# Kernel optimization log

Hardware: AMD Instinct MI355X
Metric: run time of the kernel (lower is better)

The kernel has to match this reference:

```python
import jax, jax.numpy as jnp
import numpy as np

N = 10000      # num nodes
D = 128        # in_channels == out_channels (x is fed back each step)
E1 = 320000    # edges for TAGConv
E2 = 320000    # edges for Transformer_Block
STEPS = 5      # gd_steps


def setup_inputs() -> dict:
    key = jax.random.key(0)
    ks = jax.random.split(key, 8)
    x = jax.random.normal(ks[0], (N, D), dtype=jnp.float32)
    edge_index = jax.random.randint(ks[1], (2, E1), 0, N)
    edge_index_2 = jax.random.randint(ks[2], (2, E2), 0, N)
    s = 0.02  # small init keeps the un-normalized attention unroll numerically sane
    W0 = jax.random.normal(ks[3], (D, D), dtype=jnp.float32) * s  # TAGConv lin for hop-0
    W1 = jax.random.normal(ks[4], (D, D), dtype=jnp.float32) * s  # TAGConv lin for hop-1 (A x)
    Wq = jax.random.normal(ks[5], (D, D), dtype=jnp.float32) * s
    Wk = jax.random.normal(ks[6], (D, D), dtype=jnp.float32) * s
    Wv = jax.random.normal(ks[7], (D, D), dtype=jnp.float32) * s
    return {"x": x, "edge_index": edge_index, "edge_index_2": edge_index_2,
            "W0": W0, "W1": W1, "Wq": Wq, "Wk": Wk, "Wv": Wv}


def reference(x, edge_index, edge_index_2, W0, W1, Wq, Wk, Wv):
    src, dst = edge_index[0], edge_index[1]        # message flows src -> dst
    src2, dst2 = edge_index_2[0], edge_index_2[1]

    def gd_step(h, _):
        # TAGConv(K=1, normalize=False, bias=False): W0 h + W1 (A h)
        agg = jax.ops.segment_sum(h[src], dst, num_segments=N)   # [N, D] sum over in-neighbors
        x1 = h @ W0 + agg @ W1
        # Transformer_Block (graph attention over edge_index_2, use_softmax=False):
        # alpha_ij = <q_i, k_j> on edges, out_i = sum_j alpha_ij * v_j
        Q, K, V = h @ Wq, h @ Wk, h @ Wv
        alpha = jnp.sum(Q[dst2] * K[src2], axis=-1)              # [E2] raw scores, no softmax
        x2 = jax.ops.segment_sum(alpha[:, None] * V[src2], dst2, num_segments=N)
        return x1 - x2, None

    out, _ = jax.lax.scan(gd_step, x, None, length=STEPS)
    return out
```

## Files before the change

### kernel.cpp

```cpp
#include <hip/hip_runtime.h>

#define D 128

typedef __attribute__((ext_vector_type(8))) short bf16x8;
typedef __attribute__((ext_vector_type(4))) float f32x4;

__device__ __forceinline__ unsigned short f2bf(float f) {
  union { float f; unsigned int u; } c; c.f = f;
  unsigned int u = c.u;
  unsigned int r = (u + 0x7fffu + ((u >> 16) & 1u)) >> 16;
  return (unsigned short)r;
}
__device__ __forceinline__ float bf2f(unsigned short h) {
  return __uint_as_float(((unsigned int)h) << 16);
}
__device__ __forceinline__ float bf_lo(unsigned int w) {
  return __uint_as_float(w << 16);
}
__device__ __forceinline__ float bf_hi(unsigned int w) {
  return __uint_as_float(w & 0xffff0000u);
}
__device__ __forceinline__ void split2(float a, float b, unsigned int& hi, unsigned int& lo) {
  unsigned short ha = f2bf(a), hb = f2bf(b);
  unsigned short la = f2bf(a - bf2f(ha)), lb = f2bf(b - bf2f(hb));
  hi = (unsigned int)ha | ((unsigned int)hb << 16);
  lo = (unsigned int)la | ((unsigned int)lb << 16);
}

__device__ __forceinline__ void frag_write(unsigned short* __restrict__ Afh,
                                           unsigned short* __restrict__ Afl,
                                           int t, int r, int k, float a, float b) {
  unsigned int hh, hl;
  split2(a, b, hh, hl);
  int s = k >> 5, ksub = (k & 31) >> 3, e = k & 7;
  size_t addr = ((size_t)(t * 12 + s) * 64 + r + 16 * ksub) * 8 + e;
  *(unsigned int*)&Afh[addr] = hh;
  *(unsigned int*)&Afl[addr] = hl;
}


__global__ void hist2_k(const int* __restrict__ dst1, int* __restrict__ c1, int E1,
                        const int* __restrict__ dst2, int* __restrict__ c2, int E2) {
  int e = blockIdx.x * blockDim.x + threadIdx.x;
  if (e < E1) atomicAdd(&c1[dst1[e]], 1);
  int e2 = e - E1;
  if (e2 >= 0 && e2 < E2) atomicAdd(&c2[dst2[e2]], 1);
}

__device__ void exscan_dev(int* cnt_cursor, int* rp, int n) {
  __shared__ int wsum[16];
  __shared__ int carry_s;
  const int tid = threadIdx.x;
  const int lane = tid & 63, wid = tid >> 6;
  if (tid == 0) carry_s = 0;
  __syncthreads();
  for (int base = 0; base < n; base += 1024) {
    int idx = base + tid;
    int v = (idx < n) ? cnt_cursor[idx] : 0;
    int s = v;
#pragma unroll
    for (int ofs = 1; ofs < 64; ofs <<= 1) {
      int t = __shfl_up(s, ofs);
      if (lane >= ofs) s += t;
    }
    if (lane == 63) wsum[wid] = s;
    __syncthreads();
    if (wid == 0) {
      int ws = (lane < 16) ? wsum[lane] : 0;
#pragma unroll
      for (int ofs = 1; ofs < 16; ofs <<= 1) {
        int t = __shfl_up(ws, ofs);
        if (lane >= ofs) ws += t;
      }
      if (lane < 16) wsum[lane] = ws;
    }
    __syncthreads();
    int pre = (wid > 0) ? wsum[wid - 1] : 0;
    int carry = carry_s;
    int ex = carry + pre + s - v;
    if (idx < n) { rp[idx] = ex; cnt_cursor[idx] = ex; }
    __syncthreads();
    if (tid == 1023) carry_s = carry + wsum[15];
    __syncthreads();
  }
  if (tid == 0) rp[n] = carry_s;
}

__global__ void exscan2_k(int* c1, int* r1, int* c2, int* r2, int n) {
  if (blockIdx.x == 0) exscan_dev(c1, r1, n);
  else exscan_dev(c2, r2, n);
}

__global__ void fill2_k(const int* __restrict__ src1, const int* __restrict__ dst1,
                        int* __restrict__ cur1, int* __restrict__ out1, int E1,
                        const int* __restrict__ src2, const int* __restrict__ dst2,
                        int* __restrict__ cur2, int* __restrict__ out2, int E2) {
  int e = blockIdx.x * blockDim.x + threadIdx.x;
  if (e < E1) {
    int pos = atomicAdd(&cur1[dst1[e]], 1);
    out1[pos] = src1[e];
  }
  int e2 = e - E1;
  if (e2 >= 0 && e2 < E2) {
    int pos = atomicAdd(&cur2[dst2[e2]], 1);
    out2[pos] = src2[e2];
  }
}

__global__ __launch_bounds__(256) void pre1_k(
    const float* __restrict__ Wq, const float* __restrict__ Wk,
    const float* __restrict__ W0, const float* __restrict__ W1,
    const float* __restrict__ Wv,
    float* __restrict__ M, float* __restrict__ Wc,
    int* __restrict__ cur, int twoN) {
  int gid = blockIdx.x * 256 + threadIdx.x;
  if (gid < twoN) cur[gid] = 0;
  int bx = blockIdx.x;
  if (bx < 64) {
    int r = bx * 2 + (threadIdx.x >> 7);
    int c = threadIdx.x & 127;
    float acc = 0.f;
    for (int d = 0; d < D; ++d) acc += Wq[r * D + d] * Wk[c * D + d];
    M[r * D + c] = acc;
  } else {
    int idx = (bx - 64) * 256 + threadIdx.x;
    int r = idx >> 7, c = idx & 127;
    float v;
    if (r < 128) v = W0[r * D + c];
    else if (r < 256) v = W1[(r - 128) * D + c];
    else v = -Wv[(r - 256) * D + c];
    Wc[idx] = v;
  }
}

__global__ __launch_bounds__(256) void pre2_k(const float* __restrict__ Wc,
                                              const float* __restrict__ M,
                                              float* __restrict__ WM) {
  int idx = blockIdx.x * blockDim.x + threadIdx.x;
  if (idx >= 384 * D) return;
  int r = idx >> 7, c = idx & 127;
  float acc = 0.f;
  for (int k = 0; k < D; ++k) acc += Wc[r * D + k] * M[k * D + c];
  WM[idx] = acc;
}

__global__ __launch_bounds__(256) void pre3cvt_k(
    const float* __restrict__ x,
    unsigned short* __restrict__ Afh, unsigned short* __restrict__ Afl,
    unsigned short* __restrict__ Hb, int ncvt,
    const float* __restrict__ Wc, const float* __restrict__ WM,
    const float* __restrict__ M,
    unsigned short* __restrict__ Bfh, unsigned short* __restrict__ Bfl,
    unsigned short* __restrict__ Mfh, unsigned short* __restrict__ Mfl) {
  int gid = blockIdx.x * blockDim.x + threadIdx.x;
  if (gid < ncvt) {
    int row = gid >> 6, f = (gid & 63) * 2;
    float2 v = *(const float2*)&x[row * D + f];
    frag_write(Afh, Afl, row >> 4, row & 15, f, v.x, v.y);
    unsigned int p = (unsigned int)f2bf(v.x) | ((unsigned int)f2bf(v.y) << 16);
    *(unsigned int*)&Hb[(size_t)row * D + f] = p;
    return;
  }
  int idx = gid - ncvt;
  if (idx < 16 * 12 * 512) {
    int e = idx & 7, l = (idx >> 3) & 63;
    int s = (idx >> 9) % 12, ntg = idx / (12 * 512);
    int n = ntg * 16 + (l & 15);
    int k = s * 32 + (l >> 4) * 8 + e;
    float v = (n < 128) ? Wc[k * D + n] : WM[k * D + (n - 128)];
    unsigned short h = f2bf(v);
    Bfh[idx] = h;
    Bfl[idx] = f2bf(v - bf2f(h));
  } else {
    int i2 = idx - 16 * 12 * 512;
    if (i2 >= 8 * 4 * 512) return;
    int e = i2 & 7, l = (i2 >> 3) & 63;
    int s = (i2 >> 9) & 3, ntg = i2 / (4 * 512);
    int n = ntg * 16 + (l & 15);
    int k = s * 32 + (l >> 4) * 8 + e;
    float v = M[k * D + n];
    unsigned short h = f2bf(v);
    Mfh[i2] = h;
    Mfl[i2] = f2bf(v - bf2f(h));
  }
}

__global__ __launch_bounds__(256) void agg_k(
    const float* __restrict__ h, int ldh,
    const float* __restrict__ qt,
    const unsigned short* __restrict__ Hb,
    const int* __restrict__ rp1, const int* __restrict__ s1,
    const int* __restrict__ rp2, const int* __restrict__ s2,
    unsigned short* __restrict__ Afh, unsigned short* __restrict__ Afl, int N) {
  int gw = (int)((blockIdx.x * blockDim.x + threadIdx.x) >> 6);
  if (gw >= N) return;
  const int i = __builtin_amdgcn_readfirstlane(gw);
  const int l = threadIdx.x & 63;
  const int m = l & 15, g = l >> 4;
  const int c0 = m * 8;

  float q[8];
  *(float4*)&q[0] = *(const float4*)&qt[(size_t)i * 256 + c0];
  *(float4*)&q[4] = *(const float4*)&qt[(size_t)i * 256 + c0 + 4];

  float a1[8] = {0.f, 0.f, 0.f, 0.f, 0.f, 0.f, 0.f, 0.f};
  float a2[8] = {0.f, 0.f, 0.f, 0.f, 0.f, 0.f, 0.f, 0.f};

  {
    const int lo = rp1[i], end = rp1[i + 1];
    bool nv0 = false, nv1 = false;
    int nj0 = 0, nj1 = 0;
    if (lo < end) {
      nv0 = lo + g < end;      nj0 = nv0 ? s1[lo + g] : 0;
      nv1 = lo + 4 + g < end;  nj1 = nv1 ? s1[lo + 4 + g] : 0;
    }
    for (int e = lo; e < end; e += 8) {
      int j0 = nj0, j1 = nj1;
      bool v0 = nv0, v1 = nv1;
      int en = e + 8;
      if (en < end) {
        nv0 = en + g < end;      nj0 = nv0 ? s1[en + g] : 0;
        nv1 = en + 4 + g < end;  nj1 = nv1 ? s1[en + 4 + g] : 0;
      }
      uint4 w0 = *(const uint4*)&Hb[(size_t)j0 * D + c0];
      uint4 w1 = *(const uint4*)&Hb[(size_t)j1 * D + c0];
      if (!v0) w0 = make_uint4(0u, 0u, 0u, 0u);
      if (!v1) w1 = make_uint4(0u, 0u, 0u, 0u);
      a1[0] += bf_lo(w0.x) + bf_lo(w1.x); a1[1] += bf_hi(w0.x) + bf_hi(w1.x);
      a1[2] += bf_lo(w0.y) + bf_lo(w1.y); a1[3] += bf_hi(w0.y) + bf_hi(w1.y);
      a1[4] += bf_lo(w0.z) + bf_lo(w1.z); a1[5] += bf_hi(w0.z) + bf_hi(w1.z);
      a1[6] += bf_lo(w0.w) + bf_lo(w1.w); a1[7] += bf_hi(w0.w) + bf_hi(w1.w);
    }
  }

  {
    const int lo = rp2[i], end = rp2[i + 1];
    bool nv0 = false, nv1 = false;
    int nj0 = 0, nj1 = 0;
    if (lo < end) {
      nv0 = lo + g < end;      nj0 = nv0 ? s2[lo + g] : 0;
      nv1 = lo + 4 + g < end;  nj1 = nv1 ? s2[lo + 4 + g] : 0;
    }
    for (int e = lo; e < end; e += 8) {
      int j0 = nj0, j1 = nj1;
      bool v0 = nv0, v1 = nv1;
      int en = e + 8;
      if (en < end) {
        nv0 = en + g < end;      nj0 = nv0 ? s2[en + g] : 0;
        nv1 = en + 4 + g < end;  nj1 = nv1 ? s2[en + 4 + g] : 0;
      }
      uint4 w0 = *(const uint4*)&Hb[(size_t)j0 * D + c0];
      uint4 w1 = *(const uint4*)&Hb[(size_t)j1 * D + c0];
      if (!v0) w0 = make_uint4(0u, 0u, 0u, 0u);
      if (!v1) w1 = make_uint4(0u, 0u, 0u, 0u);
      float f0[8], f1[8];
      f0[0] = bf_lo(w0.x); f0[1] = bf_hi(w0.x); f0[2] = bf_lo(w0.y); f0[3] = bf_hi(w0.y);
      f0[4] = bf_lo(w0.z); f0[5] = bf_hi(w0.z); f0[6] = bf_lo(w0.w); f0[7] = bf_hi(w0.w);
      f1[0] = bf_lo(w1.x); f1[1] = bf_hi(w1.x); f1[2] = bf_lo(w1.y); f1[3] = bf_hi(w1.y);
      f1[4] = bf_lo(w1.z); f1[5] = bf_hi(w1.z); f1[6] = bf_lo(w1.w); f1[7] = bf_hi(w1.w);
      float p0 = q[0] * f0[0] + q[1] * f0[1] + q[2] * f0[2] + q[3] * f0[3] +
                 q[4] * f0[4] + q[5] * f0[5] + q[6] * f0[6] + q[7] * f0[7];
      float p1 = q[0] * f1[0] + q[1] * f1[1] + q[2] * f1[2] + q[3] * f1[3] +
                 q[4] * f1[4] + q[5] * f1[5] + q[6] * f1[6] + q[7] * f1[7];
#pragma unroll
      for (int ofs = 1; ofs < 16; ofs <<= 1) {
        p0 += __shfl_xor(p0, ofs);
        p1 += __shfl_xor(p1, ofs);
      }
#pragma unroll
      for (int t = 0; t < 8; ++t) a2[t] += p0 * f0[t] + p1 * f1[t];
    }
  }

#pragma unroll
  for (int t = 0; t < 8; ++t) {
    a1[t] += __shfl_xor(a1[t], 16); a1[t] += __shfl_xor(a1[t], 32);
    a2[t] += __shfl_xor(a2[t], 16); a2[t] += __shfl_xor(a2[t], 32);
  }

  if (g < 3) {
    float vals[8];
    if (g == 0) {
      *(float4*)&vals[0] = *(const float4*)&h[(size_t)i * ldh + c0];
      *(float4*)&vals[4] = *(const float4*)&h[(size_t)i * ldh + c0 + 4];
    } else if (g == 1) {
#pragma unroll
      for (int t = 0; t < 8; ++t) vals[t] = a1[t];
    } else {
#pragma unroll
      for (int t = 0; t < 8; ++t) vals[t] = a2[t];
    }
    uint4 hiw, low;
    split2(vals[0], vals[1], hiw.x, low.x);
    split2(vals[2], vals[3], hiw.y, low.y);
    split2(vals[4], vals[5], hiw.z, low.z);
    split2(vals[6], vals[7], hiw.w, low.w);
    size_t base = (((size_t)(i >> 4) * 12 + g * 4 + (m >> 2)) * 64 +
                   (i & 15) + 16 * (m & 3)) * 8;
    *(uint4*)&Afh[base] = hiw;
    *(uint4*)&Afl[base] = low;
  }
}

__global__ __launch_bounds__(256) void gemm_mfma(
    const unsigned short* __restrict__ Afh, const unsigned short* __restrict__ Afl,
    int ksteps,
    const unsigned short* __restrict__ Bfh, const unsigned short* __restrict__ Bfl,
    int outcol0, float* __restrict__ C, int ldc,
    unsigned short* __restrict__ Hb,
    int N, int ntiles, int log2ny) {
  const int w = threadIdx.x >> 6, l = threadIdx.x & 63;
  const int wr = w & 1, wc = w >> 1;

  const int nwg = gridDim.x;
  const int flat = blockIdx.x;
  const int xcd = flat & 7;
  const int qq = nwg >> 3, rr8 = nwg & 7;
  const int wgid = (xcd < rr8 ? xcd * (qq + 1) : rr8 * (qq + 1) + (xcd - rr8) * qq) + (flat >> 3);
  const int rowblk = wgid >> log2ny;
  const int panel = wgid - (rowblk << log2ny);

  const int rowbase = rowblk * 64 + wr * 32;
  const int ntg0 = panel * 4 + wc * 2;

  int t_[2];
#pragma unroll
  for (int tr = 0; tr < 2; ++tr) {
    int t = (rowbase >> 4) + tr;
    t_[tr] = (t < ntiles) ? t : (ntiles - 1);
  }

  const size_t loff = (size_t)l * 8;
  const unsigned short* ah[2];
  const unsigned short* al[2];
#pragma unroll
  for (int tr = 0; tr < 2; ++tr) {
    ah[tr] = Afh + (size_t)t_[tr] * 12 * 512 + loff;
    al[tr] = Afl + (size_t)t_[tr] * 12 * 512 + loff;
  }
  const unsigned short* bh[2];
  const unsigned short* bl[2];
#pragma unroll
  for (int nt = 0; nt < 2; ++nt) {
    bh[nt] = Bfh + (size_t)(ntg0 + nt) * ksteps * 512 + loff;
    bl[nt] = Bfl + (size_t)(ntg0 + nt) * ksteps * 512 + loff;
  }

  f32x4 acc[2][2] = {};
  for (int s = 0; s < ksteps; ++s) {
    bf16x8 Ah[2], Al[2], Bh[2], Bl[2];
#pragma unroll
    for (int tr = 0; tr < 2; ++tr) {
      Ah[tr] = *(const bf16x8*)(ah[tr] + (size_t)s * 512);
      Al[tr] = *(const bf16x8*)(al[tr] + (size_t)s * 512);
    }
#pragma unroll
    for (int nt = 0; nt < 2; ++nt) {
      Bh[nt] = *(const bf16x8*)(bh[nt] + (size_t)s * 512);
      Bl[nt] = *(const bf16x8*)(bl[nt] + (size_t)s * 512);
    }
#pragma unroll
    for (int nt = 0; nt < 2; ++nt) {
#pragma unroll
      for (int tr = 0; tr < 2; ++tr) {
        acc[tr][nt] = __builtin_amdgcn_mfma_f32_16x16x32_bf16(Ah[tr], Bh[nt], acc[tr][nt], 0, 0, 0);
        acc[tr][nt] = __builtin_amdgcn_mfma_f32_16x16x32_bf16(Ah[tr], Bl[nt], acc[tr][nt], 0, 0, 0);
        acc[tr][nt] = __builtin_amdgcn_mfma_f32_16x16x32_bf16(Al[tr], Bh[nt], acc[tr][nt], 0, 0, 0);
      }
    }
  }

  const int r4 = 4 * (l >> 4), cc = (l & 15);
#pragma unroll
  for (int tr = 0; tr < 2; ++tr) {
#pragma unroll
    for (int nt = 0; nt < 2; ++nt) {
      int col = outcol0 + (ntg0 + nt) * 16 + cc;
#pragma unroll
      for (int rr = 0; rr < 4; ++rr) {
        int row = rowbase + tr * 16 + r4 + rr;
        if (row < N) {
          float v = acc[tr][nt][rr];
          C[(size_t)row * ldc + col] = v;
          if (Hb && col < 128) Hb[(size_t)row * D + col] = f2bf(v);
        }
      }
    }
  }
}


extern "C" void kernel_launch(void* const* d_in, const int* in_sizes, int n_in,
                              void* d_out, int out_size, void* d_ws, size_t ws_size,
                              hipStream_t stream) {
  const float* x  = (const float*)d_in[0];
  const int* ei1  = (const int*)d_in[1];
  const int* ei2  = (const int*)d_in[2];
  const float* W0 = (const float*)d_in[3];
  const float* W1 = (const float*)d_in[4];
  const float* Wq = (const float*)d_in[5];
  const float* Wk = (const float*)d_in[6];
  const float* Wv = (const float*)d_in[7];

  const int N  = in_sizes[0] / D;
  const int E1 = in_sizes[1] / 2;
  const int E2 = in_sizes[2] / 2;
  const int* src1 = ei1;
  const int* dst1 = ei1 + E1;
  const int* src2 = ei2;
  const int* dst2 = ei2 + E2;
  const int TILES = (N + 15) / 16;

  float* Cbuf = (float*)d_ws;
  float* M    = Cbuf + (size_t)N * 256;
  float* Wc   = M + 16384;
  float* WM   = Wc + 49152;
  unsigned short* Afh = (unsigned short*)(WM + 49152);
  unsigned short* Afl = Afh + (size_t)TILES * 6144;
  unsigned short* Bfh = Afl + (size_t)TILES * 6144;
  unsigned short* Bfl = Bfh + 98304;
  unsigned short* Mfh = Bfl + 98304;
  unsigned short* Mfl = Mfh + 16384;
  unsigned short* Hb  = Mfl + 16384;
  int* rp1   = (int*)(Hb + (size_t)N * D);
  int* rp2   = rp1 + (N + 1);
  int* cur1  = rp2 + (N + 1);
  int* cur2  = cur1 + N;
  int* srcs1 = cur2 + N;
  int* srcs2 = srcs1 + E1;

  size_t needed = ((size_t)N * 256 + 16384 + 2 * 49152) * 4ull +
                  ((size_t)2 * TILES * 6144 + 2 * 98304 + 2 * 16384 + (size_t)N * D) * 2ull +
                  ((size_t)2 * (N + 1) + 2ull * N + E1 + E2) * 4ull;
  if (ws_size < needed) return;

  float* out = (float*)d_out;

  pre1_k<<<256, 256, 0, stream>>>(Wq, Wk, W0, W1, Wv, M, Wc, cur1, 2 * N);
  pre2_k<<<(384 * D + 255) / 256, 256, 0, stream>>>(Wc, M, WM);
  {
    int ncvt = N * 64;
    int tot = ncvt + 16 * 12 * 512 + 8 * 4 * 512;
    pre3cvt_k<<<(tot + 255) / 256, 256, 0, stream>>>(x, Afh, Afl, Hb, ncvt,
                                                     Wc, WM, M, Bfh, Bfl, Mfh, Mfl);
  }
  int ebt = (E1 + E2 + 255) / 256;
  hist2_k<<<ebt, 256, 0, stream>>>(dst1, cur1, E1, dst2, cur2, E2);
  exscan2_k<<<2, 1024, 0, stream>>>(cur1, rp1, cur2, rp2, N);
  fill2_k<<<ebt, 256, 0, stream>>>(src1, dst1, cur1, srcs1, E1,
                                   src2, dst2, cur2, srcs2, E2);

  const int gx = (N + 63) / 64;
  const int ablocks = (N * 64 + 255) / 256;

  gemm_mfma<<<gx * 2, 256, 0, stream>>>(Afh, Afl, 4, Mfh, Mfl,
                                        128, Cbuf, 256, nullptr, N, TILES, 1);

  for (int s = 0; s < 5; ++s) {
    const float* hsrc = (s == 0) ? x : Cbuf;
    const int ldh = (s == 0) ? D : 256;

    agg_k<<<ablocks, 256, 0, stream>>>(hsrc, ldh, Cbuf + 128, Hb,
                                       rp1, srcs1, rp2, srcs2, Afh, Afl, N);

    if (s == 4) {
      gemm_mfma<<<gx * 2, 256, 0, stream>>>(Afh, Afl, 12, Bfh, Bfl,
                                            0, out, D, nullptr, N, TILES, 1);
    } else {
      gemm_mfma<<<gx * 4, 256, 0, stream>>>(Afh, Afl, 12, Bfh, Bfl,
                                            0, Cbuf, 256, Hb, N, TILES, 2);
    }
  }
}
```

Measured before the change: 313.5 us.

## Merge setup kernels into fewer launches and unroll edge gathers by four

The preprocessing chain goes from seven launches to four. Independent work now shares a launch: histogram with the W*M product, prefix scans with the bf16 fragment conversion, and CSR fill with the initial Q-projection GEMM, which is pulled out into a shared device function. This cuts launch and serialization overhead between small dependent kernels. Separately, the aggregation kernel now gathers four neighbor rows per iteration instead of two, exposing more memory-level parallelism at some cost in register pressure.

```diff
diff --git a/kernel.cpp b/kernel.cpp
--- a/kernel.cpp
+++ b/kernel.cpp
@@ -38,14 +38,6 @@
   *(unsigned int*)&Afl[addr] = hl;
 }
 
-
-__global__ void hist2_k(const int* __restrict__ dst1, int* __restrict__ c1, int E1,
-                        const int* __restrict__ dst2, int* __restrict__ c2, int E2) {
-  int e = blockIdx.x * blockDim.x + threadIdx.x;
-  if (e < E1) atomicAdd(&c1[dst1[e]], 1);
-  int e2 = e - E1;
-  if (e2 >= 0 && e2 < E2) atomicAdd(&c2[dst2[e2]], 1);
-}
 
 __device__ void exscan_dev(int* cnt_cursor, int* rp, int n) {
   __shared__ int wsum[16];
@@ -86,28 +78,86 @@
   if (tid == 0) rp[n] = carry_s;
 }
 
-__global__ void exscan2_k(int* c1, int* r1, int* c2, int* r2, int n) {
-  if (blockIdx.x == 0) exscan_dev(c1, r1, n);
-  else exscan_dev(c2, r2, n);
-}
-
-__global__ void fill2_k(const int* __restrict__ src1, const int* __restrict__ dst1,
-                        int* __restrict__ cur1, int* __restrict__ out1, int E1,
-                        const int* __restrict__ src2, const int* __restrict__ dst2,
-                        int* __restrict__ cur2, int* __restrict__ out2, int E2) {
-  int e = blockIdx.x * blockDim.x + threadIdx.x;
-  if (e < E1) {
-    int pos = atomicAdd(&cur1[dst1[e]], 1);
-    out1[pos] = src1[e];
-  }
-  int e2 = e - E1;
-  if (e2 >= 0 && e2 < E2) {
-    int pos = atomicAdd(&cur2[dst2[e2]], 1);
-    out2[pos] = src2[e2];
-  }
-}
-
-__global__ __launch_bounds__(256) void pre1_k(
+__device__ void gemm_tile(
+    const unsigned short* __restrict__ Afh, const unsigned short* __restrict__ Afl,
+    int ksteps,
+    const unsigned short* __restrict__ Bfh, const unsigned short* __restrict__ Bfl,
+    int outcol0, float* __restrict__ C, int ldc,
+    unsigned short* __restrict__ Hb, int N, int ntiles, int log2ny, int wgid) {
+  const int w = threadIdx.x >> 6, l = threadIdx.x & 63;
+  const int wr = w & 1, wc = w >> 1;
+  const int rowblk = wgid >> log2ny;
+  const int panel = wgid - (rowblk << log2ny);
+  const int rowbase = rowblk * 64 + wr * 32;
+  const int ntg0 = panel * 4 + wc * 2;
+
+  int t_[2];
+#pragma unroll
+  for (int tr = 0; tr < 2; ++tr) {
+    int t = (rowbase >> 4) + tr;
+    t_[tr] = (t < ntiles) ? t : (ntiles - 1);
+  }
+
+  const size_t loff = (size_t)l * 8;
+  const unsigned short* ah[2];
+  const unsigned short* al[2];
+#pragma unroll
+  for (int tr = 0; tr < 2; ++tr) {
+    ah[tr] = Afh + (size_t)t_[tr] * 12 * 512 + loff;
+    al[tr] = Afl + (size_t)t_[tr] * 12 * 512 + loff;
+  }
+  const unsigned short* bh[2];
+  const unsigned short* bl[2];
+#pragma unroll
+  for (int nt = 0; nt < 2; ++nt) {
+    bh[nt] = Bfh + (size_t)(ntg0 + nt) * ksteps * 512 + loff;
+    bl[nt] = Bfl + (size_t)(ntg0 + nt) * ksteps * 512 + loff;
+  }
+
+  f32x4 acc[2][2] = {};
+  for (int s = 0; s < ksteps; ++s) {
+    bf16x8 Ah[2], Al[2], Bh[2], Bl[2];
+#pragma unroll
+    for (int tr = 0; tr < 2; ++tr) {
+      Ah[tr] = *(const bf16x8*)(ah[tr] + (size_t)s * 512);
+      Al[tr] = *(const bf16x8*)(al[tr] + (size_t)s * 512);
+    }
+#pragma unroll
+    for (int nt = 0; nt < 2; ++nt) {
+      Bh[nt] = *(const bf16x8*)(bh[nt] + (size_t)s * 512);
+      Bl[nt] = *(const bf16x8*)(bl[nt] + (size_t)s * 512);
+    }
+#pragma unroll
+    for (int nt = 0; nt < 2; ++nt) {
+#pragma unroll
+      for (int tr = 0; tr < 2; ++tr) {
+        acc[tr][nt] = __builtin_amdgcn_mfma_f32_16x16x32_bf16(Ah[tr], Bh[nt], acc[tr][nt], 0, 0, 0);
+        acc[tr][nt] = __builtin_amdgcn_mfma_f32_16x16x32_bf16(Ah[tr], Bl[nt], acc[tr][nt], 0, 0, 0);
+        acc[tr][nt] = __builtin_amdgcn_mfma_f32_16x16x32_bf16(Al[tr], Bh[nt], acc[tr][nt], 0, 0, 0);
+      }
+    }
+  }
+
+  const int r4 = 4 * (l >> 4), cc = (l & 15);
+#pragma unroll
+  for (int tr = 0; tr < 2; ++tr) {
+#pragma unroll
+    for (int nt = 0; nt < 2; ++nt) {
+      int col = outcol0 + (ntg0 + nt) * 16 + cc;
+#pragma unroll
+      for (int rr = 0; rr < 4; ++rr) {
+        int row = rowbase + tr * 16 + r4 + rr;
+        if (row < N) {
+          float v = acc[tr][nt][rr];
+          C[(size_t)row * ldc + col] = v;
+          if (Hb && col < 128) Hb[(size_t)row * D + col] = f2bf(v);
+        }
+      }
+    }
+  }
+}
+
+__global__ __launch_bounds__(256) void k1_pre1(
     const float* __restrict__ Wq, const float* __restrict__ Wk,
     const float* __restrict__ W0, const float* __restrict__ W1,
     const float* __restrict__ Wv,
@@ -133,18 +183,28 @@
   }
 }
 
-__global__ __launch_bounds__(256) void pre2_k(const float* __restrict__ Wc,
-                                              const float* __restrict__ M,
-                                              float* __restrict__ WM) {
-  int idx = blockIdx.x * blockDim.x + threadIdx.x;
-  if (idx >= 384 * D) return;
-  int r = idx >> 7, c = idx & 127;
-  float acc = 0.f;
-  for (int k = 0; k < D; ++k) acc += Wc[r * D + k] * M[k * D + c];
-  WM[idx] = acc;
-}
-
-__global__ __launch_bounds__(256) void pre3cvt_k(
+__global__ __launch_bounds__(256) void k2_hist_pre2(
+    const int* __restrict__ dst1, int* __restrict__ c1, int E1,
+    const int* __restrict__ dst2, int* __restrict__ c2, int E2, int ebt,
+    const float* __restrict__ Wc, const float* __restrict__ M,
+    float* __restrict__ WM) {
+  if (blockIdx.x < (unsigned)ebt) {
+    int e = blockIdx.x * 256 + threadIdx.x;
+    if (e < E1) atomicAdd(&c1[dst1[e]], 1);
+    int e2 = e - E1;
+    if (e2 >= 0 && e2 < E2) atomicAdd(&c2[dst2[e2]], 1);
+  } else {
+    int idx = (blockIdx.x - ebt) * 256 + threadIdx.x;
+    if (idx >= 384 * D) return;
+    int r = idx >> 7, c = idx & 127;
+    float acc = 0.f;
+    for (int k = 0; k < D; ++k) acc += Wc[r * D + k] * M[k * D + c];
+    WM[idx] = acc;
+  }
+}
+
+__global__ __launch_bounds__(1024) void k3_scan_pre3cvt(
+    int* c1, int* r1, int* c2, int* r2, int n,
     const float* __restrict__ x,
     unsigned short* __restrict__ Afh, unsigned short* __restrict__ Afl,
     unsigned short* __restrict__ Hb, int ncvt,
@@ -152,7 +212,9 @@
     const float* __restrict__ M,
     unsigned short* __restrict__ Bfh, unsigned short* __restrict__ Bfl,
     unsigned short* __restrict__ Mfh, unsigned short* __restrict__ Mfl) {
-  int gid = blockIdx.x * blockDim.x + threadIdx.x;
+  if (blockIdx.x == 0) { exscan_dev(c1, r1, n); return; }
+  if (blockIdx.x == 1) { exscan_dev(c2, r2, n); return; }
+  int gid = (blockIdx.x - 2) * 1024 + threadIdx.x;
   if (gid < ncvt) {
     int row = gid >> 6, f = (gid & 63) * 2;
     float2 v = *(const float2*)&x[row * D + f];
@@ -165,9 +227,9 @@
   if (idx < 16 * 12 * 512) {
     int e = idx & 7, l = (idx >> 3) & 63;
     int s = (idx >> 9) % 12, ntg = idx / (12 * 512);
-    int n = ntg * 16 + (l & 15);
+    int n2 = ntg * 16 + (l & 15);
     int k = s * 32 + (l >> 4) * 8 + e;
-    float v = (n < 128) ? Wc[k * D + n] : WM[k * D + (n - 128)];
+    float v = (n2 < 128) ? Wc[k * D + n2] : WM[k * D + (n2 - 128)];
     unsigned short h = f2bf(v);
     Bfh[idx] = h;
     Bfl[idx] = f2bf(v - bf2f(h));
@@ -176,12 +238,37 @@
     if (i2 >= 8 * 4 * 512) return;
     int e = i2 & 7, l = (i2 >> 3) & 63;
     int s = (i2 >> 9) & 3, ntg = i2 / (4 * 512);
-    int n = ntg * 16 + (l & 15);
+    int n2 = ntg * 16 + (l & 15);
     int k = s * 32 + (l >> 4) * 8 + e;
-    float v = M[k * D + n];
+    float v = M[k * D + n2];
     unsigned short h = f2bf(v);
     Mfh[i2] = h;
     Mfl[i2] = f2bf(v - bf2f(h));
+  }
+}
+
+__global__ __launch_bounds__(256) void k4_fill_qtgemm(
+    const int* __restrict__ src1, const int* __restrict__ dst1,
+    int* __restrict__ cur1, int* __restrict__ out1, int E1,
+    const int* __restrict__ src2, const int* __restrict__ dst2,
+    int* __restrict__ cur2, int* __restrict__ out2, int E2, int ebt,
+    const unsigned short* __restrict__ Afh, const unsigned short* __restrict__ Afl,
+    const unsigned short* __restrict__ Mfh, const unsigned short* __restrict__ Mfl,
+    float* __restrict__ Cbuf, int N, int ntiles) {
+  if (blockIdx.x < (unsigned)ebt) {
+    int e = blockIdx.x * 256 + threadIdx.x;
+    if (e < E1) {
+      int pos = atomicAdd(&cur1[dst1[e]], 1);
+      out1[pos] = src1[e];
+    }
+    int e2 = e - E1;
+    if (e2 >= 0 && e2 < E2) {
+      int pos = atomicAdd(&cur2[dst2[e2]], 1);
+      out2[pos] = src2[e2];
+    }
+  } else {
+    gemm_tile(Afh, Afl, 4, Mfh, Mfl, 128, Cbuf, 256, nullptr, N, ntiles, 1,
+              blockIdx.x - ebt);
   }
 }
 
@@ -208,67 +295,83 @@
 
   {
     const int lo = rp1[i], end = rp1[i + 1];
-    bool nv0 = false, nv1 = false;
-    int nj0 = 0, nj1 = 0;
-    if (lo < end) {
-      nv0 = lo + g < end;      nj0 = nv0 ? s1[lo + g] : 0;
-      nv1 = lo + 4 + g < end;  nj1 = nv1 ? s1[lo + 4 + g] : 0;
-    }
-    for (int e = lo; e < end; e += 8) {
-      int j0 = nj0, j1 = nj1;
-      bool v0 = nv0, v1 = nv1;
-      int en = e + 8;
+    int nj[4]; bool nv[4];
+#pragma unroll
+    for (int u = 0; u < 4; ++u) {
+      int ee = lo + 4 * u + g;
+      nv[u] = ee < end; nj[u] = nv[u] ? s1[ee] : 0;
+    }
+    for (int e = lo; e < end; e += 16) {
+      int j[4]; bool v[4];
+#pragma unroll
+      for (int u = 0; u < 4; ++u) { j[u] = nj[u]; v[u] = nv[u]; }
+      int en = e + 16;
       if (en < end) {
-        nv0 = en + g < end;      nj0 = nv0 ? s1[en + g] : 0;
-        nv1 = en + 4 + g < end;  nj1 = nv1 ? s1[en + 4 + g] : 0;
-      }
-      uint4 w0 = *(const uint4*)&Hb[(size_t)j0 * D + c0];
-      uint4 w1 = *(const uint4*)&Hb[(size_t)j1 * D + c0];
-      if (!v0) w0 = make_uint4(0u, 0u, 0u, 0u);
-      if (!v1) w1 = make_uint4(0u, 0u, 0u, 0u);
-      a1[0] += bf_lo(w0.x) + bf_lo(w1.x); a1[1] += bf_hi(w0.x) + bf_hi(w1.x);
-      a1[2] += bf_lo(w0.y) + bf_lo(w1.y); a1[3] += bf_hi(w0.y) + bf_hi(w1.y);
-      a1[4] += bf_lo(w0.z) + bf_lo(w1.z); a1[5] += bf_hi(w0.z) + bf_hi(w1.z);
-      a1[6] += bf_lo(w0.w) + bf_lo(w1.w); a1[7] += bf_hi(w0.w) + bf_hi(w1.w);
+#pragma unroll
+        for (int u = 0; u < 4; ++u) {
+          int ee = en + 4 * u + g;
+          nv[u] = ee < end; nj[u] = nv[u] ? s1[ee] : 0;
+        }
+      }
+      uint4 w[4];
+#pragma unroll
+      for (int u = 0; u < 4; ++u)
+        w[u] = *(const uint4*)&Hb[(size_t)j[u] * D + c0];
+#pragma unroll
+      for (int u = 0; u < 4; ++u) {
+        if (!v[u]) w[u] = make_uint4(0u, 0u, 0u, 0u);
+        a1[0] += bf_lo(w[u].x); a1[1] += bf_hi(w[u].x);
+        a1[2] += bf_lo(w[u].y); a1[3] += bf_hi(w[u].y);
+        a1[4] += bf_lo(w[u].z); a1[5] += bf_hi(w[u].z);
+        a1[6] += bf_lo(w[u].w); a1[7] += bf_hi(w[u].w);
+      }
     }
   }
 
   {
     const int lo = rp2[i], end = rp2[i + 1];
-    bool nv0 = false, nv1 = false;
-    int nj0 = 0, nj1 = 0;
-    if (lo < end) {
-      nv0 = lo + g < end;      nj0 = nv0 ? s2[lo + g] : 0;
-      nv1 = lo + 4 + g < end;  nj1 = nv1 ? s2[lo + 4 + g] : 0;
-    }
-    for (int e = lo; e < end; e += 8) {
-      int j0 = nj0, j1 = nj1;
-      bool v0 = nv0, v1 = nv1;
-      int en = e + 8;
+    int nj[4]; bool nv[4];
+#pragma unroll
+    for (int u = 0; u < 4; ++u) {
+      int ee = lo + 4 * u + g;
+      nv[u] = ee < end; nj[u] = nv[u] ? s2[ee] : 0;
+    }
+    for (int e = lo; e < end; e += 16) {
+      int j[4]; bool v[4];
+#pragma unroll
+      for (int u = 0; u < 4; ++u) { j[u] = nj[u]; v[u] = nv[u]; }
+      int en = e + 16;
       if (en < end) {
-        nv0 = en + g < end;      nj0 = nv0 ? s2[en + g] : 0;
-        nv1 = en + 4 + g < end;  nj1 = nv1 ? s2[en + 4 + g] : 0;
-      }
-      uint4 w0 = *(const uint4*)&Hb[(size_t)j0 * D + c0];
-      uint4 w1 = *(const uint4*)&Hb[(size_t)j1 * D + c0];
-      if (!v0) w0 = make_uint4(0u, 0u, 0u, 0u);
-      if (!v1) w1 = make_uint4(0u, 0u, 0u, 0u);
-      float f0[8], f1[8];
-      f0[0] = bf_lo(w0.x); f0[1] = bf_hi(w0.x); f0[2] = bf_lo(w0.y); f0[3] = bf_hi(w0.y);
-      f0[4] = bf_lo(w0.z); f0[5] = bf_hi(w0.z); f0[6] = bf_lo(w0.w); f0[7] = bf_hi(w0.w);
-      f1[0] = bf_lo(w1.x); f1[1] = bf_hi(w1.x); f1[2] = bf_lo(w1.y); f1[3] = bf_hi(w1.y);
-      f1[4] = bf_lo(w1.z); f1[5] = bf_hi(w1.z); f1[6] = bf_lo(w1.w); f1[7] = bf_hi(w1.w);
-      float p0 = q[0] * f0[0] + q[1] * f0[1] + q[2] * f0[2] + q[3] * f0[3] +
-                 q[4] * f0[4] + q[5] * f0[5] + q[6] * f0[6] + q[7] * f0[7];
-      float p1 = q[0] * f1[0] + q[1] * f1[1] + q[2] * f1[2] + q[3] * f1[3] +
-                 q[4] * f1[4] + q[5] * f1[5] + q[6] * f1[6] + q[7] * f1[7];
+#pragma unroll
+        for (int u = 0; u < 4; ++u) {
+          int ee = en + 4 * u + g;
+          nv[u] = ee < end; nj[u] = nv[u] ? s2[ee] : 0;
+        }
+      }
+      uint4 w[4];
+#pragma unroll
+      for (int u = 0; u < 4; ++u)
+        w[u] = *(const uint4*)&Hb[(size_t)j[u] * D + c0];
+      float fv[4][8]; float p[4];
+#pragma unroll
+      for (int u = 0; u < 4; ++u) {
+        if (!v[u]) w[u] = make_uint4(0u, 0u, 0u, 0u);
+        fv[u][0] = bf_lo(w[u].x); fv[u][1] = bf_hi(w[u].x);
+        fv[u][2] = bf_lo(w[u].y); fv[u][3] = bf_hi(w[u].y);
+        fv[u][4] = bf_lo(w[u].z); fv[u][5] = bf_hi(w[u].z);
+        fv[u][6] = bf_lo(w[u].w); fv[u][7] = bf_hi(w[u].w);
+        p[u] = q[0] * fv[u][0] + q[1] * fv[u][1] + q[2] * fv[u][2] + q[3] * fv[u][3] +
+               q[4] * fv[u][4] + q[5] * fv[u][5] + q[6] * fv[u][6] + q[7] * fv[u][7];
+      }
 #pragma unroll
       for (int ofs = 1; ofs < 16; ofs <<= 1) {
-        p0 += __shfl_xor(p0, ofs);
-        p1 += __shfl_xor(p1, ofs);
-      }
-#pragma unroll
-      for (int t = 0; t < 8; ++t) a2[t] += p0 * f0[t] + p1 * f1[t];
+#pragma unroll
+        for (int u = 0; u < 4; ++u) p[u] += __shfl_xor(p[u], ofs);
+      }
+#pragma unroll
+      for (int u = 0; u < 4; ++u)
+#pragma unroll
+        for (int t = 0; t < 8; ++t) a2[t] += p[u] * fv[u][t];
     }
   }
 
@@ -307,86 +410,13 @@
     int ksteps,
     const unsigned short* __restrict__ Bfh, const unsigned short* __restrict__ Bfl,
     int outcol0, float* __restrict__ C, int ldc,
-    unsigned short* __restrict__ Hb,
-    int N, int ntiles, int log2ny) {
-  const int w = threadIdx.x >> 6, l = threadIdx.x & 63;
-  const int wr = w & 1, wc = w >> 1;
-
+    unsigned short* __restrict__ Hb, int N, int ntiles, int log2ny) {
   const int nwg = gridDim.x;
   const int flat = blockIdx.x;
   const int xcd = flat & 7;
   const int qq = nwg >> 3, rr8 = nwg & 7;
   const int wgid = (xcd < rr8 ? xcd * (qq + 1) : rr8 * (qq + 1) + (xcd - rr8) * qq) + (flat >> 3);
-  const int rowblk = wgid >> log2ny;
-  const int panel = wgid - (rowblk << log2ny);
-
-  const int rowbase = rowblk * 64 + wr * 32;
-  const int ntg0 = panel * 4 + wc * 2;
-
-  int t_[2];
-#pragma unroll
-  for (int tr = 0; tr < 2; ++tr) {
-    int t = (rowbase >> 4) + tr;
-    t_[tr] = (t < ntiles) ? t : (ntiles - 1);
-  }
-
-  const size_t loff = (size_t)l * 8;
-  const unsigned short* ah[2];
-  const unsigned short* al[2];
-#pragma unroll
-  for (int tr = 0; tr < 2; ++tr) {
-    ah[tr] = Afh + (size_t)t_[tr] * 12 * 512 + loff;
-    al[tr] = Afl + (size_t)t_[tr] * 12 * 512 + loff;
-  }
-  const unsigned short* bh[2];
-  const unsigned short* bl[2];
-#pragma unroll
-  for (int nt = 0; nt < 2; ++nt) {
-    bh[nt] = Bfh + (size_t)(ntg0 + nt) * ksteps * 512 + loff;
-    bl[nt] = Bfl + (size_t)(ntg0 + nt) * ksteps * 512 + loff;
-  }
-
-  f32x4 acc[2][2] = {};
-  for (int s = 0; s < ksteps; ++s) {
-    bf16x8 Ah[2], Al[2], Bh[2], Bl[2];
-#pragma unroll
-    for (int tr = 0; tr < 2; ++tr) {
-      Ah[tr] = *(const bf16x8*)(ah[tr] + (size_t)s * 512);
-      Al[tr] = *(const bf16x8*)(al[tr] + (size_t)s * 512);
-    }
-#pragma unroll
-    for (int nt = 0; nt < 2; ++nt) {
-      Bh[nt] = *(const bf16x8*)(bh[nt] + (size_t)s * 512);
-      Bl[nt] = *(const bf16x8*)(bl[nt] + (size_t)s * 512);
-    }
-#pragma unroll
-    for (int nt = 0; nt < 2; ++nt) {
-#pragma unroll
-      for (int tr = 0; tr < 2; ++tr) {
-        acc[tr][nt] = __builtin_amdgcn_mfma_f32_16x16x32_bf16(Ah[tr], Bh[nt], acc[tr][nt], 0, 0, 0);
-        acc[tr][nt] = __builtin_amdgcn_mfma_f32_16x16x32_bf16(Ah[tr], Bl[nt], acc[tr][nt], 0, 0, 0);
-        acc[tr][nt] = __builtin_amdgcn_mfma_f32_16x16x32_bf16(Al[tr], Bh[nt], acc[tr][nt], 0, 0, 0);
-      }
-    }
-  }
-
-  const int r4 = 4 * (l >> 4), cc = (l & 15);
-#pragma unroll
-  for (int tr = 0; tr < 2; ++tr) {
-#pragma unroll
-    for (int nt = 0; nt < 2; ++nt) {
-      int col = outcol0 + (ntg0 + nt) * 16 + cc;
-#pragma unroll
-      for (int rr = 0; rr < 4; ++rr) {
-        int row = rowbase + tr * 16 + r4 + rr;
-        if (row < N) {
-          float v = acc[tr][nt][rr];
-          C[(size_t)row * ldc + col] = v;
-          if (Hb && col < 128) Hb[(size_t)row * D + col] = f2bf(v);
-        }
-      }
-    }
-  }
+  gemm_tile(Afh, Afl, ksteps, Bfh, Bfl, outcol0, C, ldc, Hb, N, ntiles, log2ny, wgid);
 }
 
 
@@ -436,25 +466,21 @@
 
   float* out = (float*)d_out;
 
-  pre1_k<<<256, 256, 0, stream>>>(Wq, Wk, W0, W1, Wv, M, Wc, cur1, 2 * N);
-  pre2_k<<<(384 * D + 255) / 256, 256, 0, stream>>>(Wc, M, WM);
-  {
-    int ncvt = N * 64;
-    int tot = ncvt + 16 * 12 * 512 + 8 * 4 * 512;
-    pre3cvt_k<<<(tot + 255) / 256, 256, 0, stream>>>(x, Afh, Afl, Hb, ncvt,
-                                                     Wc, WM, M, Bfh, Bfl, Mfh, Mfl);
-  }
-  int ebt = (E1 + E2 + 255) / 256;
-  hist2_k<<<ebt, 256, 0, stream>>>(dst1, cur1, E1, dst2, cur2, E2);
-  exscan2_k<<<2, 1024, 0, stream>>>(cur1, rp1, cur2, rp2, N);
-  fill2_k<<<ebt, 256, 0, stream>>>(src1, dst1, cur1, srcs1, E1,
-                                   src2, dst2, cur2, srcs2, E2);
-
+  const int ebt = (E1 + E2 + 255) / 256;
   const int gx = (N + 63) / 64;
   const int ablocks = (N * 64 + 255) / 256;
-
-  gemm_mfma<<<gx * 2, 256, 0, stream>>>(Afh, Afl, 4, Mfh, Mfl,
-                                        128, Cbuf, 256, nullptr, N, TILES, 1);
+  const int ncvt = N * 64;
+  const int tot3 = ncvt + 16 * 12 * 512 + 8 * 4 * 512;
+
+  k1_pre1<<<256, 256, 0, stream>>>(Wq, Wk, W0, W1, Wv, M, Wc, cur1, 2 * N);
+  k2_hist_pre2<<<ebt + 192, 256, 0, stream>>>(dst1, cur1, E1, dst2, cur2, E2, ebt,
+                                              Wc, M, WM);
+  k3_scan_pre3cvt<<<2 + (tot3 + 1023) / 1024, 1024, 0, stream>>>(
+      cur1, rp1, cur2, rp2, N, x, Afh, Afl, Hb, ncvt,
+      Wc, WM, M, Bfh, Bfl, Mfh, Mfl);
+  k4_fill_qtgemm<<<ebt + gx * 2, 256, 0, stream>>>(
+      src1, dst1, cur1, srcs1, E1, src2, dst2, cur2, srcs2, E2, ebt,
+      Afh, Afl, Mfh, Mfl, Cbuf, N, TILES);
 
   for (int s = 0; s < 5; ++s) {
     const float* hsrc = (s == 0) ? x : Cbuf;
```

New measurement: 298.1 us. 1.05x faster.
